# Kernel optimization log

Hardware: AMD Instinct MI355X
Metric: run time of the kernel (lower is better)

The kernel has to match this reference:

```python
import jax, jax.numpy as jnp
import numpy as np

V, B, T, D, H = 32000, 64, 256, 512, 1024


def setup_inputs() -> dict:
    key = jax.random.key(0)
    ks = jax.random.split(key, 8)
    s = lambda i, shape: (jax.random.normal(ks[i], shape, jnp.float32) * 0.02)
    return {
        "y": jax.random.randint(ks[0], (B, T), 0, V),
        "hidden": jnp.zeros((B, H), jnp.float32),
        "emb_table": s(1, (V, D)),
        "Wx": s(2, (D, 3 * H)),
        "Wh": s(3, (H, 3 * H)),
        "bx": jnp.zeros((3 * H,), jnp.float32),
        "bh": jnp.zeros((3 * H,), jnp.float32),
        "W_out": s(4, (H, D)),
        "b_out": jnp.zeros((D,), jnp.float32),
    }


def _gru_step(h, x, Wx, Wh, bx, bh):
    # PyTorch GRUCell semantics: r,z gates, candidate n with r gating the
    # recurrent contribution (including its bias term).
    gx = x @ Wx + bx          # [B, 3H]
    gh = h @ Wh + bh          # [B, 3H]
    xr, xz, xn = jnp.split(gx, 3, axis=-1)
    hr, hz, hn = jnp.split(gh, 3, axis=-1)
    r = jax.nn.sigmoid(xr + hr)
    z = jax.nn.sigmoid(xz + hz)
    n = jnp.tanh(xn + r * hn)
    return (1.0 - z) * n + z * h


def reference(y, hidden, emb_table, Wx, Wh, bx, bh, W_out, b_out):
    emb = emb_table[y]                       # [B, T, D] token embedding lookup

    def step(h, x_t):                        # x_t: [B, D]
        h2 = _gru_step(h, x_t, Wx, Wh, bx, bh)
        return h2, h2

    _, outs = jax.lax.scan(step, hidden, jnp.swapaxes(emb, 0, 1))  # [T, B, H]
    out = jnp.swapaxes(outs, 0, 1)           # [B, T, H] decoder hiddens
    logits = jnp.tanh(out @ W_out + b_out)   # [B, T, D]; dropout_rate=0 -> identity
    return logits
```

## Files before the change

kernel.cpp:

```cpp
#include <hip/hip_runtime.h>
#include <stdint.h>

typedef unsigned short u16;
typedef unsigned int u32;
typedef __attribute__((ext_vector_type(4))) unsigned int u32x4;
typedef __attribute__((ext_vector_type(4))) float f32x4;
typedef __attribute__((ext_vector_type(8))) __bf16 bf16x8;

#define MFMA16(a, b, c) __builtin_amdgcn_mfma_f32_16x16x32_bf16((a), (b), (c), 0, 0, 0)

__device__ __forceinline__ u16 f2b(float f) {
  union { float f; unsigned u; } v; v.f = f;
  unsigned r = v.u + 0x7FFFu + ((v.u >> 16) & 1u);
  return (u16)(r >> 16);
}
__device__ __forceinline__ float b2f(u16 h) {
  union { unsigned u; float f; } v; v.u = ((unsigned)h) << 16;
  return v.f;
}
__device__ __forceinline__ float sigm(float x) { return 1.0f / (1.0f + __expf(-x)); }
__device__ __forceinline__ float tanh_fast(float x) {
  x = fminf(fmaxf(x, -15.0f), 15.0f);
  float t = __expf(2.0f * x);
  return (t - 1.0f) / (t + 1.0f);
}

template <int OFF>
__device__ __forceinline__ u32x4 ld16_sc(const u16* p) {
  u32x4 r;
  asm volatile("global_load_dwordx4 %0, %1, off offset:%2 sc0 sc1"
               : "=v"(r) : "v"(p), "i"(OFF));
  return r;
}
__device__ __forceinline__ void st16_sc(u16* p, u32x4 v) {
  asm volatile("global_store_dwordx4 %0, %1, off sc0 sc1"
               :: "v"(p), "v"(v) : "memory");
}
__device__ __forceinline__ void st4_sc(u32* p, u32 v) {
  asm volatile("global_store_dword %0, %1, off sc0 sc1"
               :: "v"(p), "v"(v) : "memory");
}
__device__ __forceinline__ u32 ld4_sc(const u32* p) {
  u32 r;
  asm volatile("global_load_dword %0, %1, off sc0 sc1\n\t"
               "s_waitcnt vmcnt(0)"
               : "=v"(r) : "v"(p) : "memory");
  return r;
}


__global__ void transpose_cvt(const float* __restrict__ src, u16* __restrict__ dst,
                              int R, int C) {
  __shared__ float tile[32][33];
  const int c0 = blockIdx.x * 32, r0 = blockIdx.y * 32;
  const int tx = threadIdx.x, ty = threadIdx.y;
  for (int i = ty; i < 32; i += 8)
    tile[i][tx] = src[(size_t)(r0 + i) * C + (c0 + tx)];
  __syncthreads();
  for (int i = ty; i < 32; i += 8)
    dst[(size_t)(c0 + i) * R + (r0 + tx)] = f2b(tile[tx][i]);
}

__global__ void gather_cast(const int* __restrict__ y, const float* __restrict__ tab,
                            u16* __restrict__ A) {
  const int idx = blockIdx.x * 256 + threadIdx.x;
  const int m = idx >> 7;
  const int d0 = (idx & 127) << 2;
  const float4 v = *reinterpret_cast<const float4*>(tab + (size_t)y[m] * 512 + d0);
  ushort4 o;
  o.x = f2b(v.x); o.y = f2b(v.y); o.z = f2b(v.z); o.w = f2b(v.w);
  *reinterpret_cast<ushort4*>(A + (size_t)m * 512 + d0) = o;
}

__global__ void cast_h0_blocked(const float* __restrict__ h, u16* __restrict__ dst) {
  const int i = blockIdx.x * 256 + threadIdx.x;
  const int b = i >> 10, n = i & 1023;
  const int r = b >> 4, ii = b & 15, g = n >> 4, j = n & 15;
  dst[((size_t)r * 64 + g) * 256 + ii * 16 + j] = f2b(h[(size_t)b * 1024 + n]);
}

template <int EPI>
__global__ __launch_bounds__(256, 2) void gemm_bt(
    const u16* __restrict__ A, const u16* __restrict__ Bt,
    const float* __restrict__ bias, void* __restrict__ Cout,
    int M, int N, int K) {
  __shared__ u16 As[4096], Bs[4096];
  const int tid = threadIdx.x, lane = tid & 63, w = tid >> 6;
  const int wm = w >> 1, wn = w & 1, c = lane & 15, hq = lane >> 4;
  const int m0 = blockIdx.y * 128, n0 = blockIdx.x * 128;
  f32x4 acc[4][4] = {};

  const int slot0 = tid, slot1 = 256 + tid;
  const int r0_ = slot0 >> 2, ko0 = (slot0 & 3) << 3;
  const int r1_ = slot1 >> 2, ko1 = (slot1 & 3) << 3;

  for (int k0 = 0; k0 < K; k0 += 32) {
    const u32x4 a0 = *(const u32x4*)(A + (size_t)(m0 + r0_) * K + k0 + ko0);
    const u32x4 a1 = *(const u32x4*)(A + (size_t)(m0 + r1_) * K + k0 + ko1);
    const u32x4 b0 = *(const u32x4*)(Bt + (size_t)(n0 + r0_) * K + k0 + ko0);
    const u32x4 b1 = *(const u32x4*)(Bt + (size_t)(n0 + r1_) * K + k0 + ko1);
    __syncthreads();
    *(u32x4*)(As + r0_ * 32 + ko0) = a0;
    *(u32x4*)(As + r1_ * 32 + ko1) = a1;
    *(u32x4*)(Bs + r0_ * 32 + ko0) = b0;
    *(u32x4*)(Bs + r1_ * 32 + ko1) = b1;
    __syncthreads();
    u32x4 af[4], bf[4];
#pragma unroll
    for (int i = 0; i < 4; ++i) {
      af[i] = *(const u32x4*)(As + (wm * 64 + i * 16 + c) * 32 + hq * 8);
      bf[i] = *(const u32x4*)(Bs + (wn * 64 + i * 16 + c) * 32 + hq * 8);
    }
#pragma unroll
    for (int mi = 0; mi < 4; ++mi)
#pragma unroll
      for (int ni = 0; ni < 4; ++ni)
        acc[mi][ni] = MFMA16(__builtin_bit_cast(bf16x8, af[mi]),
                             __builtin_bit_cast(bf16x8, bf[ni]), acc[mi][ni]);
  }

#pragma unroll
  for (int ni = 0; ni < 4; ++ni) {
    const int col = n0 + wn * 64 + ni * 16 + c;
    const float bv = bias[col];
#pragma unroll
    for (int mi = 0; mi < 4; ++mi) {
#pragma unroll
      for (int i = 0; i < 4; ++i) {
        const int m = m0 + wm * 64 + mi * 16 + hq * 4 + i;
        const float v = acc[mi][ni][i] + bv;
        if (EPI == 0) {
          const int dr = (m & 255) * 64 + (m >> 8);
          ((u16*)Cout)[(size_t)dr * N + col] = f2b(v);
        } else {
          const int dr = (m & 63) * 256 + (m >> 6);
          ((float*)Cout)[(size_t)dr * N + col] = tanh_fast(v);
        }
      }
    }
  }
}

__global__ __launch_bounds__(256, 1) void scan_kernel(
    const u16* __restrict__ wh_t,
    const float* __restrict__ bh,
    const float* __restrict__ h0,
    const u16* __restrict__ gx,
    u16* __restrict__ hbuf,
    u16* __restrict__ outs,
    u32* __restrict__ tags) {
  __shared__ u16 whs[96 * 512];
  __shared__ float red[2][3][3][256];
  __shared__ __align__(16) u16 htile[16][16];
  const int g = blockIdx.x >> 2, r = blockIdx.x & 3;
  const int tid = threadIdx.x, lane = tid & 63, s = tid >> 6;
  const int c = lane & 15, hq = lane >> 4;
  const int gcol = g * 16 + c;
  const int row0 = r * 16;

  for (int fb = s; fb < 96; fb += 4) {
    const int ss = fb / 24, kk = (fb % 24) / 3, ct = fb % 3;
    const int n = ct * 1024 + g * 16 + c;
    const int k = ss * 256 + kk * 32 + hq * 8;
    *(u32x4*)(whs + fb * 512 + lane * 8) =
        *(const u32x4*)(wh_t + (size_t)n * 1024 + k);
  }
  float bhv[3], hprev[4];
  u16 gxr[4][3];
  if (s == 0) {
#pragma unroll
    for (int ct = 0; ct < 3; ++ct) bhv[ct] = bh[ct * 1024 + gcol];
#pragma unroll
    for (int i = 0; i < 4; ++i)
      hprev[i] = h0[(size_t)(row0 + hq * 4 + i) * 1024 + gcol];
    const u16* gp = gx + gcol;
#pragma unroll
    for (int i = 0; i < 4; ++i) {
      const int b = row0 + hq * 4 + i;
      gxr[i][0] = gp[(size_t)b * 3072];
      gxr[i][1] = gp[(size_t)b * 3072 + 1024];
      gxr[i][2] = gp[(size_t)b * 3072 + 2048];
    }
  }
  __syncthreads();

  for (int t = 0; t < 256; ++t) {
    if (t > 0 && lane < 16) {
      const u32* tp = tags + (((size_t)(t & 1) * 4 + r) * 64 + s * 16 + lane) * 32;
      while (__ballot(ld4_sc(tp) < (u32)t)) {}
    }

    u32x4 af[8];
    {
      const u16* ap0 = hbuf + (((size_t)(t & 1) * 4 + r) * 64 + s * 16 + (hq >> 1)) * 256 +
                       c * 16 + (hq & 1) * 8;
      const u16* ap1 = ap0 + 2048;
      af[0] = ld16_sc<0>(ap0);    af[1] = ld16_sc<1024>(ap0);
      af[2] = ld16_sc<2048>(ap0); af[3] = ld16_sc<3072>(ap0);
      af[4] = ld16_sc<0>(ap1);    af[5] = ld16_sc<1024>(ap1);
      af[6] = ld16_sc<2048>(ap1); af[7] = ld16_sc<3072>(ap1);
    }
    asm volatile("s_waitcnt vmcnt(0)" ::: "memory");
    __builtin_amdgcn_sched_barrier(0);

    f32x4 acc[3] = {};
#pragma unroll
    for (int kk = 0; kk < 8; ++kk) {
      const int fb = (s * 8 + kk) * 3;
      const u32x4 b0 = *(const u32x4*)(whs + (fb + 0) * 512 + lane * 8);
      const u32x4 b1 = *(const u32x4*)(whs + (fb + 1) * 512 + lane * 8);
      const u32x4 b2 = *(const u32x4*)(whs + (fb + 2) * 512 + lane * 8);
      const bf16x8 a = __builtin_bit_cast(bf16x8, af[kk]);
      acc[0] = MFMA16(a, __builtin_bit_cast(bf16x8, b0), acc[0]);
      acc[1] = MFMA16(a, __builtin_bit_cast(bf16x8, b1), acc[1]);
      acc[2] = MFMA16(a, __builtin_bit_cast(bf16x8, b2), acc[2]);
    }

    if (s > 0) {
#pragma unroll
      for (int ct = 0; ct < 3; ++ct)
        *(f32x4*)&red[t & 1][s - 1][ct][lane * 4] = acc[ct];
    }
    __syncthreads();

    if (s == 0) {
      f32x4 a0 = acc[0], a1 = acc[1], a2 = acc[2];
#pragma unroll
      for (int j = 0; j < 3; ++j) {
        a0 += *(const f32x4*)&red[t & 1][j][0][lane * 4];
        a1 += *(const f32x4*)&red[t & 1][j][1][lane * 4];
        a2 += *(const f32x4*)&red[t & 1][j][2][lane * 4];
      }
#pragma unroll
      for (int i = 0; i < 4; ++i) {
        const float xr = b2f(gxr[i][0]);
        const float xz = b2f(gxr[i][1]);
        const float xn = b2f(gxr[i][2]);
        const float rr = sigm(xr + a0[i] + bhv[0]);
        const float zz = sigm(xz + a1[i] + bhv[1]);
        const float nn = tanh_fast(xn + rr * (a2[i] + bhv[2]));
        const float hnew = (1.0f - zz) * nn + zz * hprev[i];
        hprev[i] = hnew;
        htile[hq * 4 + i][c] = f2b(hnew);
      }
      asm volatile("s_waitcnt lgkmcnt(0)" ::: "memory");
      __builtin_amdgcn_sched_barrier(0);
      u32x4 hv;
      if (lane < 32) {
        hv = *(const u32x4*)((const u16*)htile + lane * 8);
        st16_sc(hbuf + (((size_t)((t + 1) & 1) * 4 + r) * 64 + g) * 256 + lane * 8, hv);
      }
      asm volatile("s_waitcnt vmcnt(0)" ::: "memory");
      if (lane == 0)
        st4_sc(tags + (((size_t)((t + 1) & 1) * 4 + r) * 64 + g) * 32, (u32)(t + 1));
      if (lane < 32) {
        const int row = row0 + (lane >> 1), c8 = (lane & 1) * 8;
        *(u32x4*)(outs + ((size_t)t * 64 + row) * 1024 + g * 16 + c8) = hv;
      }
      if (t < 255) {
        const u16* gp = gx + (size_t)(t + 1) * 64 * 3072 + gcol;
#pragma unroll
        for (int i = 0; i < 4; ++i) {
          const int b = row0 + hq * 4 + i;
          gxr[i][0] = gp[(size_t)b * 3072];
          gxr[i][1] = gp[(size_t)b * 3072 + 1024];
          gxr[i][2] = gp[(size_t)b * 3072 + 2048];
        }
      }
    }
  }
}

extern "C" void kernel_launch(void* const* d_in, const int* in_sizes, int n_in,
                              void* d_out, int out_size, void* d_ws, size_t ws_size,
                              hipStream_t stream) {
  (void)in_sizes; (void)n_in; (void)out_size; (void)ws_size;
  const int* y = (const int*)d_in[0];
  const float* hidden = (const float*)d_in[1];
  const float* emb = (const float*)d_in[2];
  const float* Wx = (const float*)d_in[3];
  const float* Wh = (const float*)d_in[4];
  const float* bx = (const float*)d_in[5];
  const float* bh = (const float*)d_in[6];
  const float* Wout = (const float*)d_in[7];
  const float* bout = (const float*)d_in[8];

  char* p = (char*)d_ws;
  u16* wx_t = (u16*)p; p += (size_t)3072 * 512 * 2;
  u16* wh_t = (u16*)p; p += (size_t)3072 * 1024 * 2;
  u16* wo_t = (u16*)p; p += (size_t)512 * 1024 * 2;
  u16* aemb = (u16*)p; p += (size_t)16384 * 512 * 2;
  u16* gx   = (u16*)p; p += (size_t)16384 * 3072 * 2;
  u16* outs = (u16*)p; p += (size_t)16384 * 1024 * 2;
  u16* hbuf = (u16*)p; p += (size_t)2 * 4 * 64 * 256 * 2;
  u32* tags = (u32*)p;

  hipMemsetAsync(tags, 0, 2 * 4 * 64 * 32 * sizeof(u32), stream);
  transpose_cvt<<<dim3(96, 16), dim3(32, 8), 0, stream>>>(Wx, wx_t, 512, 3072);
  transpose_cvt<<<dim3(96, 32), dim3(32, 8), 0, stream>>>(Wh, wh_t, 1024, 3072);
  transpose_cvt<<<dim3(16, 32), dim3(32, 8), 0, stream>>>(Wout, wo_t, 1024, 512);
  gather_cast<<<dim3(8192), dim3(256), 0, stream>>>(y, emb, aemb);
  cast_h0_blocked<<<dim3(256), dim3(256), 0, stream>>>(hidden, hbuf);

  gemm_bt<0><<<dim3(24, 128), dim3(256), 0, stream>>>(aemb, wx_t, bx, (void*)gx,
                                                      16384, 3072, 512);
  scan_kernel<<<dim3(256), dim3(256), 0, stream>>>(wh_t, bh, hidden, gx,
                                                   hbuf, outs, tags);
  gemm_bt<1><<<dim3(4, 128), dim3(256), 0, stream>>>(outs, wo_t, bout,
                                                     d_out, 16384, 512, 1024);
}
```

Before: 925.9 us.

## Embed step tags in hidden-state words to drop separate flag polling

Each published hidden value becomes a 32-bit word holding the bf16 value in its high half and the step counter in its low half. Consumers poll the data itself until every tag matches, then unpack the bf16 halves into MFMA operands. This removes the separate tag store, the store-then-flag ordering wait, and the tag-then-data double round trip on the serial recurrence path. In exchange each poll loads twice as many bytes and spends ALU on validation and repacking.

After: 1.417 ms. 1.53x slower.

```diff
diff --git a/kernel.cpp b/kernel.cpp
--- a/kernel.cpp
+++ b/kernel.cpp
@@ -26,26 +26,15 @@
 }
 
 template <int OFF>
-__device__ __forceinline__ u32x4 ld16_sc(const u16* p) {
+__device__ __forceinline__ u32x4 ld16_sc(const void* p) {
   u32x4 r;
   asm volatile("global_load_dwordx4 %0, %1, off offset:%2 sc0 sc1"
                : "=v"(r) : "v"(p), "i"(OFF));
   return r;
 }
-__device__ __forceinline__ void st16_sc(u16* p, u32x4 v) {
+__device__ __forceinline__ void st16_sc(void* p, u32x4 v) {
   asm volatile("global_store_dwordx4 %0, %1, off sc0 sc1"
                :: "v"(p), "v"(v) : "memory");
-}
-__device__ __forceinline__ void st4_sc(u32* p, u32 v) {
-  asm volatile("global_store_dword %0, %1, off sc0 sc1"
-               :: "v"(p), "v"(v) : "memory");
-}
-__device__ __forceinline__ u32 ld4_sc(const u32* p) {
-  u32 r;
-  asm volatile("global_load_dword %0, %1, off sc0 sc1\n\t"
-               "s_waitcnt vmcnt(0)"
-               : "=v"(r) : "v"(p) : "memory");
-  return r;
 }
 
 
@@ -72,11 +61,12 @@
   *reinterpret_cast<ushort4*>(A + (size_t)m * 512 + d0) = o;
 }
 
-__global__ void cast_h0_blocked(const float* __restrict__ h, u16* __restrict__ dst) {
+__global__ void cast_h0_blocked(const float* __restrict__ h, u32* __restrict__ dst) {
   const int i = blockIdx.x * 256 + threadIdx.x;
   const int b = i >> 10, n = i & 1023;
   const int r = b >> 4, ii = b & 15, g = n >> 4, j = n & 15;
-  dst[((size_t)r * 64 + g) * 256 + ii * 16 + j] = f2b(h[(size_t)b * 1024 + n]);
+  dst[((size_t)r * 64 + g) * 256 + ii * 16 + j] =
+      ((u32)f2b(h[(size_t)b * 1024 + n]) << 16);
 }
 
 template <int EPI>
@@ -146,12 +136,11 @@
     const float* __restrict__ bh,
     const float* __restrict__ h0,
     const u16* __restrict__ gx,
-    u16* __restrict__ hbuf,
-    u16* __restrict__ outs,
-    u32* __restrict__ tags) {
+    u32* __restrict__ hx,
+    u16* __restrict__ outs) {
   __shared__ u16 whs[96 * 512];
   __shared__ float red[2][3][3][256];
-  __shared__ __align__(16) u16 htile[16][16];
+  __shared__ u32 htile[256];
   const int g = blockIdx.x >> 2, r = blockIdx.x & 3;
   const int tid = threadIdx.x, lane = tid & 63, s = tid >> 6;
   const int c = lane & 15, hq = lane >> 4;
@@ -185,23 +174,43 @@
   __syncthreads();
 
   for (int t = 0; t < 256; ++t) {
-    if (t > 0 && lane < 16) {
-      const u32* tp = tags + (((size_t)(t & 1) * 4 + r) * 64 + s * 16 + lane) * 32;
-      while (__ballot(ld4_sc(tp) < (u32)t)) {}
-    }
-
+    u32x4 d[16];
+    {
+      const u32* ap0 = hx + (((size_t)(t & 1) * 4 + r) * 64 + s * 16 + (hq >> 1)) * 256 +
+                       c * 16 + (hq & 1) * 8;
+      const u32* ap1 = ap0 + 1024;
+      const u32* ap2 = ap0 + 2048;
+      const u32* ap3 = ap0 + 3072;
+      const u32 texp = (u32)t;
+      while (true) {
+        d[0]  = ld16_sc<0>(ap0); d[1]  = ld16_sc<16>(ap0);
+        d[2]  = ld16_sc<2048>(ap0); d[3]  = ld16_sc<2064>(ap0);
+        d[4]  = ld16_sc<0>(ap1); d[5]  = ld16_sc<16>(ap1);
+        d[6]  = ld16_sc<2048>(ap1); d[7]  = ld16_sc<2064>(ap1);
+        d[8]  = ld16_sc<0>(ap2); d[9]  = ld16_sc<16>(ap2);
+        d[10] = ld16_sc<2048>(ap2); d[11] = ld16_sc<2064>(ap2);
+        d[12] = ld16_sc<0>(ap3); d[13] = ld16_sc<16>(ap3);
+        d[14] = ld16_sc<2048>(ap3); d[15] = ld16_sc<2064>(ap3);
+        asm volatile("s_waitcnt vmcnt(0)" ::: "memory");
+        __builtin_amdgcn_sched_barrier(0);
+        u32 bad = 0;
+#pragma unroll
+        for (int q = 0; q < 16; ++q)
+#pragma unroll
+          for (int e = 0; e < 4; ++e) bad |= (d[q][e] ^ texp);
+        if (__ballot((bad & 0xFFFFu) != 0) == 0) break;
+        __builtin_amdgcn_s_sleep(1);
+      }
+    }
     u32x4 af[8];
-    {
-      const u16* ap0 = hbuf + (((size_t)(t & 1) * 4 + r) * 64 + s * 16 + (hq >> 1)) * 256 +
-                       c * 16 + (hq & 1) * 8;
-      const u16* ap1 = ap0 + 2048;
-      af[0] = ld16_sc<0>(ap0);    af[1] = ld16_sc<1024>(ap0);
-      af[2] = ld16_sc<2048>(ap0); af[3] = ld16_sc<3072>(ap0);
-      af[4] = ld16_sc<0>(ap1);    af[5] = ld16_sc<1024>(ap1);
-      af[6] = ld16_sc<2048>(ap1); af[7] = ld16_sc<3072>(ap1);
-    }
-    asm volatile("s_waitcnt vmcnt(0)" ::: "memory");
-    __builtin_amdgcn_sched_barrier(0);
+#pragma unroll
+    for (int kk = 0; kk < 8; ++kk) {
+      const u32x4 lo = d[kk * 2], hi = d[kk * 2 + 1];
+      af[kk][0] = (lo[1] & 0xFFFF0000u) | (lo[0] >> 16);
+      af[kk][1] = (lo[3] & 0xFFFF0000u) | (lo[2] >> 16);
+      af[kk][2] = (hi[1] & 0xFFFF0000u) | (hi[0] >> 16);
+      af[kk][3] = (hi[3] & 0xFFFF0000u) | (hi[2] >> 16);
+    }
 
     f32x4 acc[3] = {};
 #pragma unroll
@@ -241,22 +250,17 @@
         const float nn = tanh_fast(xn + rr * (a2[i] + bhv[2]));
         const float hnew = (1.0f - zz) * nn + zz * hprev[i];
         hprev[i] = hnew;
-        htile[hq * 4 + i][c] = f2b(hnew);
+        htile[(hq * 4 + i) * 16 + c] = ((u32)f2b(hnew) << 16) | (u32)(t + 1);
       }
       asm volatile("s_waitcnt lgkmcnt(0)" ::: "memory");
       __builtin_amdgcn_sched_barrier(0);
-      u32x4 hv;
-      if (lane < 32) {
-        hv = *(const u32x4*)((const u16*)htile + lane * 8);
-        st16_sc(hbuf + (((size_t)((t + 1) & 1) * 4 + r) * 64 + g) * 256 + lane * 8, hv);
-      }
-      asm volatile("s_waitcnt vmcnt(0)" ::: "memory");
-      if (lane == 0)
-        st4_sc(tags + (((size_t)((t + 1) & 1) * 4 + r) * 64 + g) * 32, (u32)(t + 1));
-      if (lane < 32) {
-        const int row = row0 + (lane >> 1), c8 = (lane & 1) * 8;
-        *(u32x4*)(outs + ((size_t)t * 64 + row) * 1024 + g * 16 + c8) = hv;
-      }
+      const u32x4 hv = *(const u32x4*)&htile[lane * 4];
+      st16_sc(hx + (((size_t)((t + 1) & 1) * 4 + r) * 64 + g) * 256 + lane * 4, hv);
+      ushort4 ob;
+      ob.x = (u16)(hv[0] >> 16); ob.y = (u16)(hv[1] >> 16);
+      ob.z = (u16)(hv[2] >> 16); ob.w = (u16)(hv[3] >> 16);
+      *(ushort4*)(outs + ((size_t)t * 64 + row0 + (lane >> 2)) * 1024 +
+                  g * 16 + (lane & 3) * 4) = ob;
       if (t < 255) {
         const u16* gp = gx + (size_t)(t + 1) * 64 * 3072 + gcol;
 #pragma unroll
@@ -292,20 +296,17 @@
   u16* aemb = (u16*)p; p += (size_t)16384 * 512 * 2;
   u16* gx   = (u16*)p; p += (size_t)16384 * 3072 * 2;
   u16* outs = (u16*)p; p += (size_t)16384 * 1024 * 2;
-  u16* hbuf = (u16*)p; p += (size_t)2 * 4 * 64 * 256 * 2;
-  u32* tags = (u32*)p;
-
-  hipMemsetAsync(tags, 0, 2 * 4 * 64 * 32 * sizeof(u32), stream);
+  u32* hx   = (u32*)p; p += (size_t)2 * 4 * 64 * 256 * 4;
+
   transpose_cvt<<<dim3(96, 16), dim3(32, 8), 0, stream>>>(Wx, wx_t, 512, 3072);
   transpose_cvt<<<dim3(96, 32), dim3(32, 8), 0, stream>>>(Wh, wh_t, 1024, 3072);
   transpose_cvt<<<dim3(16, 32), dim3(32, 8), 0, stream>>>(Wout, wo_t, 1024, 512);
   gather_cast<<<dim3(8192), dim3(256), 0, stream>>>(y, emb, aemb);
-  cast_h0_blocked<<<dim3(256), dim3(256), 0, stream>>>(hidden, hbuf);
+  cast_h0_blocked<<<dim3(256), dim3(256), 0, stream>>>(hidden, hx);
 
   gemm_bt<0><<<dim3(24, 128), dim3(256), 0, stream>>>(aemb, wx_t, bx, (void*)gx,
                                                       16384, 3072, 512);
-  scan_kernel<<<dim3(256), dim3(256), 0, stream>>>(wh_t, bh, hidden, gx,
-                                                   hbuf, outs, tags);
+  scan_kernel<<<dim3(256), dim3(256), 0, stream>>>(wh_t, bh, hidden, gx, hx, outs);
   gemm_bt<1><<<dim3(4, 128), dim3(256), 0, stream>>>(outs, wo_t, bout,
                                                      d_out, 16384, 512, 1024);
 }
```
